# Performance work log

Measured on AMD Instinct MI355X. Metric: run time of the kernel, lower is better.

## Reference

```python
import jax, jax.numpy as jnp
import numpy as np

BATCH = 65536
VEC = 512       # CLIP embedding dim
K = 1024        # num_cluster
GAMMA = 0.99
EPS = 1e-05


def setup_inputs() -> dict:
    key = jax.random.key(0)
    k1, k2, k3 = jax.random.split(key, 3)
    batch_vectors = jax.random.normal(k1, (BATCH, VEC), dtype=jnp.float32)
    weight = jax.random.normal(k2, (VEC, K), dtype=jnp.float32)        # codebook, stored (vec_size, num_cluster)
    cluster_size = jnp.ones((K,), dtype=jnp.float32)
    embed_avg = jax.random.normal(k3, (VEC, K), dtype=jnp.float32)
    return {
        "batch_vectors": batch_vectors,
        "weight": weight,
        "cluster_size": cluster_size,
        "embed_avg": embed_avg,
    }


def reference(batch_vectors, weight, cluster_size, embed_avg):
    """One minibatch_update step of clusteringEMA_torch.

    Returns the updated codebook `weight` of shape (vec_size, num_cluster).
    """
    gamma = GAMMA
    eps = EPS
    num_cluster = weight.shape[1]

    # nearest centroid: squared L2 distance has the same argmin as the L2 norm
    x2 = jnp.sum(batch_vectors * batch_vectors, axis=1, keepdims=True)   # (B,1)
    w2 = jnp.sum(weight * weight, axis=0)[None, :]                       # (1,K)
    dist2 = x2 + w2 - 2.0 * (batch_vectors @ weight)                     # (B,K)
    argmin = jnp.argmin(dist2, axis=-1)                                  # (B,)

    # per-cluster counts (one-hot sum), zeros replaced by 1
    counts = jnp.zeros((num_cluster,), dtype=batch_vectors.dtype).at[argmin].add(1.0)
    n_idx_choice = jnp.where(counts == 0, 1.0, counts)

    # EMA of cluster sizes
    new_cluster_size = gamma * cluster_size + (1.0 - gamma) * n_idx_choice

    # embed_sum = x^T @ onehot  == per-cluster sum of assigned vectors, (vec,K)
    embed_sum = jax.ops.segment_sum(batch_vectors, argmin, num_segments=num_cluster).T
    new_embed_avg = gamma * embed_avg + (1.0 - gamma) * embed_sum

    # Laplace-smoothed normalization
    n = jnp.sum(new_cluster_size)
    cs = (new_cluster_size + eps) / (n + num_cluster * eps) * n
    new_weight = new_embed_avg / cs[None, :]
    return new_weight
```

## Files before the change

kernel.cpp:

```cpp
#include <hip/hip_runtime.h>

typedef unsigned int uint;
typedef unsigned short ushort_t;
typedef unsigned long long u64;
typedef __attribute__((ext_vector_type(4))) float f32x4;
typedef __attribute__((ext_vector_type(8))) __bf16 bf16x8;
typedef __attribute__((ext_vector_type(8))) unsigned short us8;

#define BATCH 65536
#define VEC 512
#define K 1024
#define GAMMA 0.99f
#define EPS 1e-05f
#define SEG 64
#define MARGIN 0.75f

#define NKT (VEC / 32)

__device__ __forceinline__ ushort_t rtn(float f) {
    uint u = __float_as_uint(f);
    return (ushort_t)((u + 0x7FFFu + ((u >> 16) & 1u)) >> 16);
}

__device__ __forceinline__ void gl16(const void* g, void* l) {
    __builtin_amdgcn_global_load_lds(
        (const __attribute__((address_space(1))) unsigned int*)g,
        (__attribute__((address_space(3))) unsigned int*)l, 16, 0, 0);
}

__device__ __forceinline__ float dec_key(uint e) {
    uint b = (e & 0x80000000u) ? (e & 0x7FFFFFFFu) : ~e;
    return __uint_as_float(b);
}

__global__ void k_pack_w(const float* __restrict__ w, us8* __restrict__ wpk,
                         float* __restrict__ wT, float* __restrict__ w2p,
                         int* __restrict__ cc ) {
    __shared__ float lds[32][257];
    const int g = blockIdx.x;
    const int gx = g >> 4, ks = g & 15;
    const int t = threadIdx.x;

#pragma unroll
    for (int r = 0; r < 32; ++r)
        lds[r][t] = w[(size_t)(ks * 32 + r) * K + gx * 256 + t];
    __syncthreads();

    float s = 0.f;
#pragma unroll
    for (int r = 0; r < 32; ++r) { float f = lds[r][t]; s += f * f; }
    w2p[ks * K + gx * 256 + t] = s;

#pragma unroll
    for (int i = 0; i < 4; ++i) {
        const int o = i * 256 + t;
        const int lane = o & 63, ct = o >> 6;
        const int cl = ct * 16 + (lane & 15);
        const int r0 = (lane >> 4) * 8;
        us8 v;
#pragma unroll
        for (int j = 0; j < 8; ++j) v[j] = rtn(lds[r0 + j][cl]);
        wpk[(size_t)g * 1024 + o] = v;
    }

#pragma unroll
    for (int rr = 0; rr < 8; ++rr) {
        f32x4 v = {lds[rr * 4 + 0][t], lds[rr * 4 + 1][t], lds[rr * 4 + 2][t], lds[rr * 4 + 3][t]};
        *(f32x4*)&wT[(size_t)(gx * 256 + t) * VEC + ks * 32 + rr * 4] = v;
    }

    if (g < 8) cc[g * 256 + t] = 0;
    if (g == 8 && t == 0) cc[2048] = 0;
}

__launch_bounds__(512, 4)
__global__ void k_gemm(const float* __restrict__ x, const us8* __restrict__ wpk,
                       const float* __restrict__ w2p,
                       u64* __restrict__ keysA, u64* __restrict__ keysB) {
    __shared__ us8 a_lds[2][512];
    __shared__ us8 b_lds[2][1024];

    const int blk = blockIdx.x;
    const int gy = (blk & 7) * 64 + ((blk >> 3) >> 2);
    const int gx = (blk >> 3) & 3;
    const int t = threadIdx.x;
    const int lane = t & 63;
    const int wv = t >> 6;
    const int wm = wv >> 2;
    const int wn = wv & 3;

    const us8* bsrc = wpk + (size_t)gx * (NKT * 1024);

    const int al = t & 63;
    const float* xp = x + (size_t)(gy * 128 + (t >> 6) * 16 + (al & 15)) * VEC + (al >> 4) * 8;
    f32x4 av0, av1;
    auto aload = [&](int kt) {
        const float* p = xp + kt * 32;
        av0 = *(const f32x4*)p;
        av1 = *(const f32x4*)(p + 4);
    };
    auto awrite = [&](int buf) {
        us8 h;
#pragma unroll
        for (int j = 0; j < 4; ++j) { h[j] = rtn(av0[j]); h[4 + j] = rtn(av1[j]); }
        a_lds[buf][t] = h;
    };
    auto bstage = [&](int buf, int kt) {
        const us8* sb = bsrc + (size_t)kt * 1024;
        gl16(sb + t, &b_lds[buf][t]);
        gl16(sb + 512 + t, &b_lds[buf][512 + t]);
    };

    f32x4 acc[4][4];
#pragma unroll
    for (int i = 0; i < 4; ++i)
#pragma unroll
        for (int j = 0; j < 4; ++j) acc[i][j] = (f32x4){0.f, 0.f, 0.f, 0.f};

    aload(0);
    bstage(0, 0);
    awrite(0);
    asm volatile("s_waitcnt lgkmcnt(0)" ::: "memory");

    for (int tk = 0; tk < NKT; ++tk) {
        const int buf = tk & 1;
        const bool nx = (tk + 1 < NKT);
        if (nx) {
            aload(tk + 1);
            bstage(buf ^ 1, tk + 1);
            asm volatile("s_waitcnt vmcnt(4)" ::: "memory");
        } else {
            asm volatile("s_waitcnt vmcnt(0)" ::: "memory");
        }
        __builtin_amdgcn_s_barrier();

        bf16x8 bh[4];
#pragma unroll
        for (int ct = 0; ct < 4; ++ct)
            bh[ct] = __builtin_bit_cast(bf16x8, b_lds[buf][(wn * 4 + ct) * 64 + lane]);
#pragma unroll
        for (int rt = 0; rt < 4; ++rt) {
            bf16x8 ah = __builtin_bit_cast(bf16x8, a_lds[buf][(wm * 4 + rt) * 64 + lane]);
#pragma unroll
            for (int ct = 0; ct < 4; ++ct)
                acc[rt][ct] = __builtin_amdgcn_mfma_f32_16x16x32_bf16(ah, bh[ct], acc[rt][ct], 0, 0, 0);
        }

        if (nx) awrite(buf ^ 1);
        asm volatile("s_waitcnt lgkmcnt(0)" ::: "memory");
        __builtin_amdgcn_s_barrier();
    }

    const int col_base = gx * 256 + wn * 64;
    float w2c[4];
#pragma unroll
    for (int ct = 0; ct < 4; ++ct) {
        const int col = col_base + ct * 16 + (lane & 15);
        float s = 0.f;
#pragma unroll
        for (int p = 0; p < 16; ++p) s += w2p[p * K + col];
        w2c[ct] = s;
    }
    const int slot = gx * 4 + wn;

#pragma unroll
    for (int rt = 0; rt < 4; ++rt) {
#pragma unroll
        for (int reg = 0; reg < 4; ++reg) {
            u64 k1 = ~0ull, k2 = ~0ull;
#pragma unroll
            for (int ct = 0; ct < 4; ++ct) {
                float dist = w2c[ct] - 2.0f * acc[rt][ct][reg];
                uint su = __float_as_uint(dist);
                su = (su & 0x80000000u) ? ~su : (su | 0x80000000u);
                const u64 key = ((u64)su << 32) | (uint)(col_base + ct * 16 + (lane & 15));
                if (key < k1) { k2 = k1; k1 = key; }
                else if (key < k2) { k2 = key; }
            }
#pragma unroll
            for (int m = 1; m < 16; m <<= 1) {
                u64 o1 = __shfl_xor((unsigned long long)k1, m);
                u64 o2 = __shfl_xor((unsigned long long)k2, m);
                u64 lo = k1 < o1 ? k1 : o1;
                u64 hi = k1 < o1 ? o1 : k1;
                u64 mn2 = k2 < o2 ? k2 : o2;
                k1 = lo;
                k2 = hi < mn2 ? hi : mn2;
            }
            if ((lane & 15) == 0) {
                const int row = gy * 128 + wm * 64 + rt * 16 + (lane >> 4) * 4 + reg;
                keysA[(size_t)slot * BATCH + row] = k1;
                keysB[(size_t)slot * BATCH + row] = k2;
            }
        }
    }
}

__global__ void k_verify(const u64* __restrict__ keysA, const u64* __restrict__ keysB,
                         int* __restrict__ am, int* __restrict__ counts,
                         u64* __restrict__ list, int* __restrict__ listcnt,
                         float* __restrict__ esum) {
    const int r = blockIdx.x * 256 + threadIdx.x;
    f32x4 z = {0.f, 0.f, 0.f, 0.f};
    ((f32x4*)esum)[r * 2] = z;
    ((f32x4*)esum)[r * 2 + 1] = z;

    u64 m1 = ~0ull, s = ~0ull;
    int i1 = 0;
#pragma unroll
    for (int i = 0; i < 16; ++i) {
        u64 a = keysA[(size_t)i * BATCH + r];
        if (a < m1) { s = m1; m1 = a; i1 = i; }
        else if (a < s) s = a;
    }
    u64 b = keysB[(size_t)i1 * BATCH + r];
    u64 m2 = s < b ? s : b;

    const float d1 = dec_key((uint)(m1 >> 32));
    const float d2 = dec_key((uint)(m2 >> 32));
    const int c1 = (int)(uint)m1 & 1023;
    const int c2 = (int)(uint)m2 & 1023;

    if (d2 - d1 > MARGIN) {
        am[r] = c1;
        atomicAdd(&counts[c1], 1);
    } else {
        int p = atomicAdd(listcnt, 1);
        list[p] = ((u64)(uint)r << 32) | ((uint)c1 << 10) | (uint)c2;
    }
}

__launch_bounds__(256)
__global__ void k_recheck(const float* __restrict__ x, const float* __restrict__ wT,
                          const float* __restrict__ w2p, const u64* __restrict__ list,
                          const int* __restrict__ listcnt, int* __restrict__ am,
                          int* __restrict__ counts) {
    const int gwid = (blockIdx.x * 256 + threadIdx.x) >> 6;
    const int lane = threadIdx.x & 63;
    const int n = *listcnt;
    for (int idx = gwid; idx < n; idx += 1024) {
        const u64 e = list[idx];
        const int r = (int)(e >> 32);
        const int c1 = (int)((e >> 10) & 1023);
        const int c2 = (int)(e & 1023);
        const f32x4 x0 = *(const f32x4*)&x[(size_t)r * VEC + lane * 8];
        const f32x4 x1 = *(const f32x4*)&x[(size_t)r * VEC + lane * 8 + 4];
        float d[2];
        const int cc2[2] = {c1, c2};
#pragma unroll
        for (int j = 0; j < 2; ++j) {
            const int c = cc2[j];
            const f32x4 w0 = *(const f32x4*)&wT[(size_t)c * VEC + lane * 8];
            const f32x4 w1 = *(const f32x4*)&wT[(size_t)c * VEC + lane * 8 + 4];
            float p = x0[0] * w0[0] + x0[1] * w0[1] + x0[2] * w0[2] + x0[3] * w0[3]
                    + x1[0] * w1[0] + x1[1] * w1[1] + x1[2] * w1[2] + x1[3] * w1[3];
#pragma unroll
            for (int m = 1; m < 64; m <<= 1) p += __shfl_xor(p, m);
            float w2 = 0.f;
#pragma unroll
            for (int q = 0; q < 16; ++q) w2 += w2p[q * K + c];
            d[j] = w2 - 2.0f * p;
        }
        const int win = (d[0] < d[1] || (d[0] == d[1] && c1 < c2)) ? c1 : c2;
        if (lane == 0) {
            am[r] = win;
            atomicAdd(&counts[win], 1);
        }
    }
}

__global__ void k_scan(const int* __restrict__ counts,
                       const float* __restrict__ cluster_size,
                       int* __restrict__ offsets, float* __restrict__ cs) {
    __shared__ int wsum[16];
    __shared__ float fw[16];
    const int t = threadIdx.x;
    const int lane = t & 63, wid = t >> 6;
    const int c = counts[t];

    int s = c;
#pragma unroll
    for (int d = 1; d < 64; d <<= 1) {
        int o = __shfl_up(s, d);
        if (lane >= d) s += o;
    }
    float ncs = GAMMA * cluster_size[t] + (1.0f - GAMMA) * ((c == 0) ? 1.0f : (float)c);
    float fs = ncs;
#pragma unroll
    for (int d = 32; d > 0; d >>= 1) fs += __shfl_xor(fs, d);

    if (lane == 63) wsum[wid] = s;
    if (lane == 0) fw[wid] = fs;
    __syncthreads();
    if (wid == 0 && lane < 16) {
        int v = wsum[lane];
#pragma unroll
        for (int d = 1; d < 16; d <<= 1) {
            int o = __shfl_up(v, d);
            if (lane >= d) v += o;
        }
        wsum[lane] = v;
    }
    __syncthreads();
    const int base = wid ? wsum[wid - 1] : 0;
    offsets[t] = base + s - c;

    float n = 0.f;
#pragma unroll
    for (int i = 0; i < 16; ++i) n += fw[i];
    cs[t] = (ncs + EPS) / (n + (float)K * EPS) * n;
}

__global__ void k_scatter(const int* __restrict__ am, const int* __restrict__ offsets,
                          int* __restrict__ cursor, int* __restrict__ sorted,
                          int* __restrict__ sortedk) {
    const int b = blockIdx.x * blockDim.x + threadIdx.x;
    const int k = am[b];
    const int pos = atomicAdd(&cursor[k], 1);
    sorted[offsets[k] + pos] = b;
    sortedk[offsets[k] + pos] = k;
}

__launch_bounds__(512)
__global__ void k_segred(const float* __restrict__ x, const int* __restrict__ sorted,
                         const int* __restrict__ sortedk, float* __restrict__ esum) {
    __shared__ int srow[SEG];
    __shared__ int skid[SEG];
    const int b = blockIdx.x;
    const int t = threadIdx.x;
    if (t < SEG) {
        srow[t] = sorted[b * SEG + t];
        skid[t] = sortedk[b * SEG + t];
    }
    __syncthreads();

    float a = 0.f;
    int cur = skid[0];
#pragma unroll 8
    for (int i = 0; i < SEG; ++i) {
        const int k = skid[i];
        if (k != cur) {
            atomicAdd(&esum[(size_t)cur * VEC + t], a);
            a = 0.f;
            cur = k;
        }
        a += x[(size_t)srow[i] * VEC + t];
    }
    atomicAdd(&esum[(size_t)cur * VEC + t], a);
}

__launch_bounds__(256)
__global__ void k_finalize(const float* __restrict__ esum, const float* __restrict__ embed_avg,
                           const float* __restrict__ cs, float* __restrict__ out) {
    __shared__ float tile[64][65];
    const int k0 = blockIdx.x * 64;
    const int v0 = blockIdx.y * 64;
    const int c = threadIdx.x & 63;
    const int r0 = threadIdx.x >> 6;
#pragma unroll
    for (int j = 0; j < 16; ++j) {
        const int r = r0 + j * 4;
        tile[r][c] = esum[(size_t)(k0 + r) * VEC + v0 + c];
    }
    __syncthreads();
    const float csk = cs[k0 + c];
#pragma unroll
    for (int j = 0; j < 16; ++j) {
        const int r = r0 + j * 4;
        const size_t o = (size_t)(v0 + r) * K + k0 + c;
        out[o] = (GAMMA * embed_avg[o] + (1.0f - GAMMA) * tile[c][r]) / csk;
    }
}

extern "C" void kernel_launch(void* const* d_in, const int* in_sizes, int n_in,
                              void* d_out, int out_size, void* d_ws, size_t ws_size,
                              hipStream_t stream) {
    const float* x            = (const float*)d_in[0];
    const float* w            = (const float*)d_in[1];
    const float* cluster_size = (const float*)d_in[2];
    const float* embed_avg    = (const float*)d_in[3];
    float* out = (float*)d_out;

    u64*   keysA   = (u64*)d_ws;
    u64*   keysB   = keysA + (size_t)16 * BATCH;
    int*   am      = (int*)(keysB + (size_t)16 * BATCH);
    u64*   list    = (u64*)(am + BATCH);
    float* w2p     = (float*)(list + BATCH);
    float* cs      = w2p + 16 * K;
    int*   cc      = (int*)(cs + K);
    int*   counts  = cc;
    int*   cursor  = cc + K;
    int*   listcnt = cc + 2 * K;
    int*   offsets = cc + 2 * K + 64;
    int*   sorted  = offsets + K;
    int*   sortedk = sorted + BATCH;
    float* esum    = (float*)(sortedk + BATCH);
    us8*   wpk     = (us8*)(esum + (size_t)K * VEC);
    float* wT      = (float*)(wpk + (size_t)64 * 1024);

    k_pack_w<<<64, 256, 0, stream>>>(w, wpk, wT, w2p, cc);
    k_gemm<<<2048, 512, 0, stream>>>(x, wpk, w2p, keysA, keysB);
    k_verify<<<BATCH / 256, 256, 0, stream>>>(keysA, keysB, am, counts, list, listcnt, esum);
    k_recheck<<<256, 256, 0, stream>>>(x, wT, w2p, list, listcnt, am, counts);
    k_scan<<<1, K, 0, stream>>>(counts, cluster_size, offsets, cs);
    k_scatter<<<BATCH / 256, 256, 0, stream>>>(am, offsets, cursor, sorted, sortedk);
    k_segred<<<BATCH / SEG, 512, 0, stream>>>(x, sorted, sortedk, esum);
    k_finalize<<<dim3(K / 64, VEC / 64), 256, 0, stream>>>(esum, embed_avg, cs, out);
}
```

Measured before the change: 393.8 us.

## Pre-pack x to bf16 and enlarge GEMM tile to 256x256 with K=64 stages

Adds a separate kernel that converts x to bf16 in an MFMA-friendly packed layout, so the GEMM can stage both operands with direct global-to-LDS loads instead of converting in registers. The GEMM tile grows from 128 to 256 rows per block with 64-wide K steps, giving each wave 8x4 accumulators and more reuse per LDS load. The inner loop is split into phases with barriers and setprio to interleave LDS reads and MFMA across waves. This costs an extra pass that writes a bf16 copy of x, plus higher register pressure and lower occupancy.

```diff
diff --git a/kernel.cpp b/kernel.cpp
--- a/kernel.cpp
+++ b/kernel.cpp
@@ -15,7 +15,8 @@
 #define SEG 64
 #define MARGIN 0.75f
 
-#define NKT (VEC / 32)
+#define NKT (VEC / 64)
+#define TG 2048
 
 __device__ __forceinline__ ushort_t rtn(float f) {
     uint u = __float_as_uint(f);
@@ -32,122 +33,184 @@
     uint b = (e & 0x80000000u) ? (e & 0x7FFFFFFFu) : ~e;
     return __uint_as_float(b);
 }
+
+#define BC8(p) __builtin_bit_cast(bf16x8, (p))
 
 __global__ void k_pack_w(const float* __restrict__ w, us8* __restrict__ wpk,
                          float* __restrict__ wT, float* __restrict__ w2p,
                          int* __restrict__ cc ) {
     __shared__ float lds[32][257];
     const int g = blockIdx.x;
-    const int gx = g >> 4, ks = g & 15;
+    const int gx = g >> 3, kt = g & 7;
     const int t = threadIdx.x;
 
-#pragma unroll
-    for (int r = 0; r < 32; ++r)
-        lds[r][t] = w[(size_t)(ks * 32 + r) * K + gx * 256 + t];
-    __syncthreads();
-
     float s = 0.f;
 #pragma unroll
-    for (int r = 0; r < 32; ++r) { float f = lds[r][t]; s += f * f; }
-    w2p[ks * K + gx * 256 + t] = s;
-
-#pragma unroll
-    for (int i = 0; i < 4; ++i) {
-        const int o = i * 256 + t;
-        const int lane = o & 63, ct = o >> 6;
-        const int cl = ct * 16 + (lane & 15);
-        const int r0 = (lane >> 4) * 8;
-        us8 v;
-#pragma unroll
-        for (int j = 0; j < 8; ++j) v[j] = rtn(lds[r0 + j][cl]);
-        wpk[(size_t)g * 1024 + o] = v;
-    }
-
-#pragma unroll
-    for (int rr = 0; rr < 8; ++rr) {
-        f32x4 v = {lds[rr * 4 + 0][t], lds[rr * 4 + 1][t], lds[rr * 4 + 2][t], lds[rr * 4 + 3][t]};
-        *(f32x4*)&wT[(size_t)(gx * 256 + t) * VEC + ks * 32 + rr * 4] = v;
-    }
+    for (int ih = 0; ih < 2; ++ih) {
+        __syncthreads();
+#pragma unroll
+        for (int r = 0; r < 32; ++r)
+            lds[r][t] = w[(size_t)(kt * 64 + ih * 32 + r) * K + gx * 256 + t];
+        __syncthreads();
+
+#pragma unroll
+        for (int r = 0; r < 32; ++r) { float f = lds[r][t]; s += f * f; }
+
+#pragma unroll
+        for (int i = 0; i < 4; ++i) {
+            const int c = i * 256 + t;
+            const int ct = c >> 6, lane = c & 63;
+            const int cl = ct * 16 + (lane & 15);
+            const int r0 = (lane >> 4) * 8;
+            us8 v;
+#pragma unroll
+            for (int j = 0; j < 8; ++j) v[j] = rtn(lds[r0 + j][cl]);
+            wpk[(size_t)g * TG + ct * 128 + ih * 64 + lane] = v;
+        }
+
+#pragma unroll
+        for (int rr = 0; rr < 8; ++rr) {
+            f32x4 v = {lds[rr * 4 + 0][t], lds[rr * 4 + 1][t],
+                       lds[rr * 4 + 2][t], lds[rr * 4 + 3][t]};
+            *(f32x4*)&wT[(size_t)(gx * 256 + t) * VEC + kt * 64 + ih * 32 + rr * 4] = v;
+        }
+    }
+    w2p[kt * K + gx * 256 + t] = s;
 
     if (g < 8) cc[g * 256 + t] = 0;
     if (g == 8 && t == 0) cc[2048] = 0;
 }
 
-__launch_bounds__(512, 4)
-__global__ void k_gemm(const float* __restrict__ x, const us8* __restrict__ wpk,
+__global__ void k_pack_x(const float* __restrict__ x, us8* __restrict__ xpk) {
+    const int blk = blockIdx.x;
+    const int gy = blk >> 3, kt = blk & 7;
+    const int t = threadIdx.x;
+#pragma unroll
+    for (int i = 0; i < 8; ++i) {
+        const int g = i * 256 + t;
+        const int slab = g >> 7, ksub = (g >> 6) & 1, lane = g & 63;
+        const int row = gy * 256 + slab * 16 + (lane & 15);
+        const int k = kt * 64 + ksub * 32 + ((lane >> 4) << 3);
+        const f32x4 q0 = *(const f32x4*)&x[(size_t)row * VEC + k];
+        const f32x4 q1 = *(const f32x4*)&x[(size_t)row * VEC + k + 4];
+        us8 v;
+#pragma unroll
+        for (int j = 0; j < 4; ++j) { v[j] = rtn(q0[j]); v[4 + j] = rtn(q1[j]); }
+        xpk[(size_t)blk * TG + g] = v;
+    }
+}
+
+__launch_bounds__(512, 2)
+__global__ void k_gemm(const us8* __restrict__ xpk, const us8* __restrict__ wpk,
                        const float* __restrict__ w2p,
                        u64* __restrict__ keysA, u64* __restrict__ keysB) {
-    __shared__ us8 a_lds[2][512];
-    __shared__ us8 b_lds[2][1024];
+    __shared__ us8 lds[2][2 * TG];
 
     const int blk = blockIdx.x;
-    const int gy = (blk & 7) * 64 + ((blk >> 3) >> 2);
-    const int gx = (blk >> 3) & 3;
+    const int ord = blk >> 3;
+    const int gy = (blk & 7) * 32 + (ord >> 2);
+    const int gx = ord & 3;
     const int t = threadIdx.x;
     const int lane = t & 63;
     const int wv = t >> 6;
     const int wm = wv >> 2;
     const int wn = wv & 3;
 
-    const us8* bsrc = wpk + (size_t)gx * (NKT * 1024);
-
-    const int al = t & 63;
-    const float* xp = x + (size_t)(gy * 128 + (t >> 6) * 16 + (al & 15)) * VEC + (al >> 4) * 8;
-    f32x4 av0, av1;
-    auto aload = [&](int kt) {
-        const float* p = xp + kt * 32;
-        av0 = *(const f32x4*)p;
-        av1 = *(const f32x4*)(p + 4);
+    const us8* asrc = xpk + (size_t)gy * (NKT * TG);
+    const us8* bsrc = wpk + (size_t)gx * (NKT * TG);
+
+    auto stage = [&](int slot, int kt) {
+        const us8* sa = asrc + (size_t)kt * TG;
+        const us8* sb = bsrc + (size_t)kt * TG;
+#pragma unroll
+        for (int i = 0; i < 4; ++i) gl16(sa + i * 512 + t, &lds[slot][i * 512 + t]);
+#pragma unroll
+        for (int i = 0; i < 4; ++i) gl16(sb + i * 512 + t, &lds[slot][TG + i * 512 + t]);
     };
-    auto awrite = [&](int buf) {
-        us8 h;
-#pragma unroll
-        for (int j = 0; j < 4; ++j) { h[j] = rtn(av0[j]); h[4 + j] = rtn(av1[j]); }
-        a_lds[buf][t] = h;
-    };
-    auto bstage = [&](int buf, int kt) {
-        const us8* sb = bsrc + (size_t)kt * 1024;
-        gl16(sb + t, &b_lds[buf][t]);
-        gl16(sb + 512 + t, &b_lds[buf][512 + t]);
-    };
-
-    f32x4 acc[4][4];
-#pragma unroll
-    for (int i = 0; i < 4; ++i)
+
+    f32x4 acc[8][4];
+#pragma unroll
+    for (int i = 0; i < 8; ++i)
 #pragma unroll
         for (int j = 0; j < 4; ++j) acc[i][j] = (f32x4){0.f, 0.f, 0.f, 0.f};
 
-    aload(0);
-    bstage(0, 0);
-    awrite(0);
-    asm volatile("s_waitcnt lgkmcnt(0)" ::: "memory");
-
-    for (int tk = 0; tk < NKT; ++tk) {
-        const int buf = tk & 1;
-        const bool nx = (tk + 1 < NKT);
-        if (nx) {
-            aload(tk + 1);
-            bstage(buf ^ 1, tk + 1);
-            asm volatile("s_waitcnt vmcnt(4)" ::: "memory");
+    stage(0, 0);
+    stage(1, 1);
+
+    for (int kt = 0; kt < NKT; ++kt) {
+        const int buf = kt & 1;
+        if (kt >= 1 && kt + 1 < NKT) {
+            stage(buf ^ 1, kt + 1);
+            asm volatile("s_waitcnt vmcnt(8)" ::: "memory");
+        } else if (kt == 0) {
+            asm volatile("s_waitcnt vmcnt(8)" ::: "memory");
         } else {
             asm volatile("s_waitcnt vmcnt(0)" ::: "memory");
         }
         __builtin_amdgcn_s_barrier();
 
-        bf16x8 bh[4];
-#pragma unroll
-        for (int ct = 0; ct < 4; ++ct)
-            bh[ct] = __builtin_bit_cast(bf16x8, b_lds[buf][(wn * 4 + ct) * 64 + lane]);
-#pragma unroll
-        for (int rt = 0; rt < 4; ++rt) {
-            bf16x8 ah = __builtin_bit_cast(bf16x8, a_lds[buf][(wm * 4 + rt) * 64 + lane]);
-#pragma unroll
-            for (int ct = 0; ct < 4; ++ct)
-                acc[rt][ct] = __builtin_amdgcn_mfma_f32_16x16x32_bf16(ah, bh[ct], acc[rt][ct], 0, 0, 0);
-        }
-
-        if (nx) awrite(buf ^ 1);
+        const us8* A = &lds[buf][0];
+        const us8* B = &lds[buf][TG];
+        bf16x8 ah[8], b0, b1;
+
+#pragma unroll
+        for (int rt = 0; rt < 8; ++rt) ah[rt] = BC8(A[(wm * 8 + rt) * 128 + lane]);
+        b0 = BC8(B[(wn * 4 + 0) * 128 + lane]);
+        b1 = BC8(B[(wn * 4 + 1) * 128 + lane]);
+        __builtin_amdgcn_s_barrier();
         asm volatile("s_waitcnt lgkmcnt(0)" ::: "memory");
+        __builtin_amdgcn_sched_barrier(0);
+        __builtin_amdgcn_s_setprio(1);
+#pragma unroll
+        for (int rt = 0; rt < 8; ++rt) {
+            acc[rt][0] = __builtin_amdgcn_mfma_f32_16x16x32_bf16(ah[rt], b0, acc[rt][0], 0, 0, 0);
+            acc[rt][1] = __builtin_amdgcn_mfma_f32_16x16x32_bf16(ah[rt], b1, acc[rt][1], 0, 0, 0);
+        }
+        __builtin_amdgcn_s_setprio(0);
+        __builtin_amdgcn_s_barrier();
+
+        b0 = BC8(B[(wn * 4 + 2) * 128 + lane]);
+        b1 = BC8(B[(wn * 4 + 3) * 128 + lane]);
+        __builtin_amdgcn_s_barrier();
+        asm volatile("s_waitcnt lgkmcnt(0)" ::: "memory");
+        __builtin_amdgcn_sched_barrier(0);
+        __builtin_amdgcn_s_setprio(1);
+#pragma unroll
+        for (int rt = 0; rt < 8; ++rt) {
+            acc[rt][2] = __builtin_amdgcn_mfma_f32_16x16x32_bf16(ah[rt], b0, acc[rt][2], 0, 0, 0);
+            acc[rt][3] = __builtin_amdgcn_mfma_f32_16x16x32_bf16(ah[rt], b1, acc[rt][3], 0, 0, 0);
+        }
+        __builtin_amdgcn_s_setprio(0);
+        __builtin_amdgcn_s_barrier();
+
+#pragma unroll
+        for (int rt = 0; rt < 8; ++rt) ah[rt] = BC8(A[(wm * 8 + rt) * 128 + 64 + lane]);
+        b0 = BC8(B[(wn * 4 + 0) * 128 + 64 + lane]);
+        b1 = BC8(B[(wn * 4 + 1) * 128 + 64 + lane]);
+        __builtin_amdgcn_s_barrier();
+        asm volatile("s_waitcnt lgkmcnt(0)" ::: "memory");
+        __builtin_amdgcn_sched_barrier(0);
+        __builtin_amdgcn_s_setprio(1);
+#pragma unroll
+        for (int rt = 0; rt < 8; ++rt) {
+            acc[rt][0] = __builtin_amdgcn_mfma_f32_16x16x32_bf16(ah[rt], b0, acc[rt][0], 0, 0, 0);
+            acc[rt][1] = __builtin_amdgcn_mfma_f32_16x16x32_bf16(ah[rt], b1, acc[rt][1], 0, 0, 0);
+        }
+        __builtin_amdgcn_s_setprio(0);
+        __builtin_amdgcn_s_barrier();
+
+        b0 = BC8(B[(wn * 4 + 2) * 128 + 64 + lane]);
+        b1 = BC8(B[(wn * 4 + 3) * 128 + 64 + lane]);
+        __builtin_amdgcn_s_barrier();
+        asm volatile("s_waitcnt lgkmcnt(0)" ::: "memory");
+        __builtin_amdgcn_sched_barrier(0);
+        __builtin_amdgcn_s_setprio(1);
+#pragma unroll
+        for (int rt = 0; rt < 8; ++rt) {
+            acc[rt][2] = __builtin_amdgcn_mfma_f32_16x16x32_bf16(ah[rt], b0, acc[rt][2], 0, 0, 0);
+            acc[rt][3] = __builtin_amdgcn_mfma_f32_16x16x32_bf16(ah[rt], b1, acc[rt][3], 0, 0, 0);
+        }
+        __builtin_amdgcn_s_setprio(0);
         __builtin_amdgcn_s_barrier();
     }
 
@@ -158,13 +221,13 @@
         const int col = col_base + ct * 16 + (lane & 15);
         float s = 0.f;
 #pragma unroll
-        for (int p = 0; p < 16; ++p) s += w2p[p * K + col];
+        for (int p = 0; p < 8; ++p) s += w2p[p * K + col];
         w2c[ct] = s;
     }
     const int slot = gx * 4 + wn;
 
 #pragma unroll
-    for (int rt = 0; rt < 4; ++rt) {
+    for (int rt = 0; rt < 8; ++rt) {
 #pragma unroll
         for (int reg = 0; reg < 4; ++reg) {
             u64 k1 = ~0ull, k2 = ~0ull;
@@ -188,7 +251,7 @@
                 k2 = hi < mn2 ? hi : mn2;
             }
             if ((lane & 15) == 0) {
-                const int row = gy * 128 + wm * 64 + rt * 16 + (lane >> 4) * 4 + reg;
+                const int row = gy * 256 + wm * 128 + rt * 16 + (lane >> 4) * 4 + reg;
                 keysA[(size_t)slot * BATCH + row] = k1;
                 keysB[(size_t)slot * BATCH + row] = k2;
             }
@@ -258,7 +321,7 @@
             for (int m = 1; m < 64; m <<= 1) p += __shfl_xor(p, m);
             float w2 = 0.f;
 #pragma unroll
-            for (int q = 0; q < 16; ++q) w2 += w2p[q * K + c];
+            for (int q = 0; q < 8; ++q) w2 += w2p[q * K + c];
             d[j] = w2 - 2.0f * p;
         }
         const int win = (d[0] < d[1] || (d[0] == d[1] && c1 < c2)) ? c1 : c2;
@@ -386,7 +449,7 @@
     int*   am      = (int*)(keysB + (size_t)16 * BATCH);
     u64*   list    = (u64*)(am + BATCH);
     float* w2p     = (float*)(list + BATCH);
-    float* cs      = w2p + 16 * K;
+    float* cs      = w2p + 8 * K;
     int*   cc      = (int*)(cs + K);
     int*   counts  = cc;
     int*   cursor  = cc + K;
@@ -396,10 +459,12 @@
     int*   sortedk = sorted + BATCH;
     float* esum    = (float*)(sortedk + BATCH);
     us8*   wpk     = (us8*)(esum + (size_t)K * VEC);
-    float* wT      = (float*)(wpk + (size_t)64 * 1024);
-
-    k_pack_w<<<64, 256, 0, stream>>>(w, wpk, wT, w2p, cc);
-    k_gemm<<<2048, 512, 0, stream>>>(x, wpk, w2p, keysA, keysB);
+    float* wT      = (float*)(wpk + (size_t)32 * TG);
+    us8*   xpk     = (us8*)(wT + (size_t)K * VEC);
+
+    k_pack_w<<<32, 256, 0, stream>>>(w, wpk, wT, w2p, cc);
+    k_pack_x<<<2048, 256, 0, stream>>>(x, xpk);
+    k_gemm<<<1024, 512, 0, stream>>>(xpk, wpk, w2p, keysA, keysB);
     k_verify<<<BATCH / 256, 256, 0, stream>>>(keysA, keysB, am, counts, list, listcnt, esum);
     k_recheck<<<256, 256, 0, stream>>>(x, wT, w2p, list, listcnt, am, counts);
     k_scan<<<1, K, 0, stream>>>(counts, cluster_size, offsets, cs);
```

Result: slower. 413.8 us (+5.1%).
